# Kernel tuning notes

Hardware: AMD Instinct MI355X
Metric: run time of the kernel (lower is better)

Reference implementation:

```python
import jax, jax.numpy as jnp
import numpy as np

EPS = 1e-7
K_CURV = 1.0                       # init_curvature buffer
HOPFIELD_DIM = 128
BETA = 1.0 / HOPFIELD_DIM ** 0.5   # default beta = 1/sqrt(hopfield_dim)


def _to_tangent0(x):
    # prepend zero time coordinate, clip max norm to 3.5
    zeros = jnp.zeros(x.shape[:-1] + (1,), dtype=x.dtype)
    x = jnp.concatenate([zeros, x], axis=-1)
    n = jnp.linalg.norm(x, axis=-1, keepdims=True)
    factor = jnp.minimum(3.5 / (n + EPS), 1.0)
    return x * factor


def _linner(u, v):
    # Minkowski (Lorentz) inner product: -u0*v0 + sum_i ui*vi
    return -u[..., 0] * v[..., 0] + jnp.sum(u[..., 1:] * v[..., 1:], axis=-1)


def _expmap0(u, k):
    # exp map at hyperboloid origin; u has zero time component
    sk = jnp.sqrt(k)
    xs = u[..., 1:]
    n = jnp.maximum(jnp.linalg.norm(xs, axis=-1, keepdims=True), EPS)
    t = n / sk
    return jnp.concatenate([sk * jnp.cosh(t), sk * jnp.sinh(t) * xs / n], axis=-1)


def _logmap(x, y, k):
    # log map of y in tangent space at x
    xy = _linner(x, y)[..., None]
    dist = jnp.sqrt(k) * jnp.arccosh(jnp.maximum(-xy / k, 1.0 + EPS))
    nomin = y + (xy / k) * x
    denom = jnp.sqrt(jnp.maximum(_linner(nomin, nomin)[..., None], EPS))
    return dist * nomin / denom


def _expmap(x, u, k):
    # exp map of tangent vector u at base point x
    sk = jnp.sqrt(k)
    un = jnp.sqrt(jnp.maximum(_linner(u, u)[..., None], EPS))
    t = un / sk
    return jnp.cosh(t) * x + sk * jnp.sinh(t) * u / un


def _logmap0(x, k):
    # log map at origin; time component of the result is zero
    sk = jnp.sqrt(k)
    xs = x[..., 1:]
    n = jnp.maximum(jnp.linalg.norm(xs, axis=-1, keepdims=True), EPS)
    dist = sk * jnp.arccosh(jnp.maximum(x[..., :1] / sk, 1.0 + EPS))
    return jnp.concatenate([jnp.zeros_like(x[..., :1]), dist * xs / n], axis=-1)


def setup_inputs() -> dict:
    key = jax.random.key(0)
    k1, k2, k3, k4, k5 = jax.random.split(key, 5)
    N, M, D_MEM, D_H, D_OUT = 1024, 2048, 512, 128, 128
    return {
        "queries": jax.random.normal(k1, (N, D_H), dtype=jnp.float32),
        "keys": jax.random.normal(k2, (M, D_MEM), dtype=jnp.float32),
        "values": jax.random.normal(k3, (M, D_MEM), dtype=jnp.float32),
        "W_K": jax.random.normal(k4, (D_MEM, D_H), dtype=jnp.float32) * 0.05,
        "W_V": jax.random.normal(k5, (D_H, D_OUT), dtype=jnp.float32) * 0.05,
    }


def reference(queries, keys, values, W_K, W_V):
    k = K_CURV
    Q = _expmap0(_to_tangent0(queries), k)              # [N, D+1]
    K = _expmap0(_to_tangent0(keys @ W_K), k)           # [M, D+1]
    V = _expmap0(_to_tangent0((values @ W_K) @ W_V), k) # [M, D+1]
    sim = _linner(Q[:, None, :], K[None, :, :])         # [N, M]
    alpha = jax.nn.softmax(-BETA * sim, axis=-1)        # [N, M]
    log_values = _logmap(Q[:, None, :], V[None, :, :], k)  # [N, M, D+1]
    tangent_mean = jnp.sum(alpha[..., None] * log_values, axis=1)  # [N, D+1]
    z = _expmap(Q, tangent_mean, k)
    return _logmap0(z, k)[..., 1:]                      # [N, D]
```

## Files before the change

kernel.cpp:

```cpp
#include <hip/hip_runtime.h>
#include <math.h>

#define EPSF 1e-7f
#define BETA_F 0.08838834764831845f

typedef __attribute__((ext_vector_type(8))) short bf8_t;
typedef __attribute__((ext_vector_type(4))) float f32x4;

#define WS_QT    0
#define WS_LQ    1024
#define WS_KT    2048
#define WS_VTM   4096
#define WS_LV    6144
#define WS_QS    8192
#define WS_QHI   139264
#define WS_QLO   204800
#define WS_KHI   270336
#define WS_KLO   401408
#define WS_VHI   532480
#define WS_VLO   663552
#define WS_VTHI  794624
#define WS_VTLO  925696
#define WS_WKT0  1056768
#define WS_WKT1  1089536
#define WS_WKT2  1122304
#define WS_WVT0  1155072
#define WS_WVT1  1163264
#define WS_WVT2  1171456
#define WS_PART  1179648

__device__ __forceinline__ float wave_sum(float v) {
#pragma unroll
  for (int off = 32; off > 0; off >>= 1) v += __shfl_xor(v, off);
  return v;
}
__device__ __forceinline__ unsigned short f2bf(float x) {
  unsigned int u = __float_as_uint(x);
  u += 0x7FFFu + ((u >> 16) & 1u);
  return (unsigned short)(u >> 16);
}
__device__ __forceinline__ float bf2f(unsigned short h) {
  return __uint_as_float(((unsigned int)h) << 16);
}
__device__ __forceinline__ void split3(float x, unsigned short& s0, unsigned short& s1,
                                       unsigned short& s2) {
  s0 = f2bf(x);
  float r1 = x - bf2f(s0);
  s1 = f2bf(r1);
  s2 = f2bf(r1 - bf2f(s1));
}
__device__ __forceinline__ bf8_t ld8(const unsigned short* p) {
  return __builtin_bit_cast(bf8_t, *(const uint4*)p);
}
__device__ __forceinline__ f32x4 mfma16(bf8_t a, bf8_t b, f32x4 c) {
  return __builtin_amdgcn_mfma_f32_16x16x32_bf16(a, b, c, 0, 0, 0);
}

__global__ void prep_q(const float* __restrict__ queries, float* __restrict__ Qs,
                       float* __restrict__ qt, float* __restrict__ lqv,
                       unsigned int* __restrict__ Qhi, unsigned int* __restrict__ Qlo) {
  int i = blockIdx.x;
  int lane = threadIdx.x;
  float2 r = ((const float2*)(queries + (size_t)i * 128))[lane];
  float s2 = wave_sum(r.x * r.x + r.y * r.y);
  float n = sqrtf(s2);
  float f = fminf(3.5f / (n + EPSF), 1.0f);
  float t = fmaxf(n * f, EPSF);
  float coef = sinhf(t) / t * f;
  float ch = coshf(t);
  float x0 = coef * r.x, x1 = coef * r.y;
  ((float2*)(Qs + (size_t)i * 128))[lane] = make_float2(x0, x1);
  unsigned short h0 = f2bf(x0), h1 = f2bf(x1);
  Qhi[i * 64 + lane] = (unsigned)h0 | ((unsigned)h1 << 16);
  unsigned short g0 = f2bf(x0 - bf2f(h0)), g1 = f2bf(x1 - bf2f(h1));
  Qlo[i * 64 + lane] = (unsigned)g0 | ((unsigned)g1 << 16);
  if (lane == 0) {
    qt[i] = ch;
    lqv[i] = coef * coef * s2 - ch * ch;
  }
}

__global__ void convert_w(const float* __restrict__ WK, const float* __restrict__ WV,
                          unsigned short* __restrict__ WKT0, unsigned short* __restrict__ WKT1,
                          unsigned short* __restrict__ WKT2,
                          unsigned short* __restrict__ WVT0, unsigned short* __restrict__ WVT1,
                          unsigned short* __restrict__ WVT2) {
  int t = blockIdx.x * 256 + threadIdx.x;
  if (t < 65536) {
    int n = t >> 9, k = t & 511;
    unsigned short a, b, c;
    split3(WK[k * 128 + n], a, b, c);
    WKT0[t] = a; WKT1[t] = b; WKT2[t] = c;
  } else {
    int t2 = t - 65536;
    int n = t2 >> 7, k = t2 & 127;
    unsigned short a, b, c;
    split3(WV[k * 128 + n], a, b, c);
    WVT0[t2] = a; WVT1[t2] = b; WVT2[t2] = c;
  }
}

__launch_bounds__(512, 2)
__global__ void prep_kv(const float* __restrict__ keys, const float* __restrict__ values,
                        const unsigned short* __restrict__ WKT0,
                        const unsigned short* __restrict__ WKT1,
                        const unsigned short* __restrict__ WKT2,
                        const unsigned short* __restrict__ WVT0,
                        const unsigned short* __restrict__ WVT1,
                        const unsigned short* __restrict__ WVT2,
                        unsigned short* __restrict__ Khi, unsigned short* __restrict__ Klo,
                        float* __restrict__ kt,
                        unsigned short* __restrict__ Vhi, unsigned short* __restrict__ Vlo,
                        unsigned short* __restrict__ VThi, unsigned short* __restrict__ VTlo,
                        float* __restrict__ vt, float* __restrict__ lv) {
  int tid = threadIdx.x, wv = tid >> 6, lane = tid & 63;
  int l15 = lane & 15, lh = lane >> 4;
  int b = blockIdx.x;
  bool isK = b < 128;
  int r0 = (b & 127) * 16;
  const float* src = isK ? keys : values;

  __shared__ __align__(16) float ldsD[16][132];
  __shared__ __align__(16) unsigned short v1p[3][16][128];
  __shared__ __align__(16) float ldsD2[16][132];
  __shared__ __align__(16) float ldsT[128][17];

  f32x4 acc = f32x4{0, 0, 0, 0};
  const float* arow = src + (size_t)(r0 + l15) * 512 + lh * 8;
  size_t bbase = (size_t)(wv * 16 + l15) * 512 + lh * 8;

  float4 pa0[2], pa1[2];
  bf8_t pb0[2], pb1[2], pb2[2];
  pa0[0] = *(const float4*)(arow);
  pa1[0] = *(const float4*)(arow + 4);
  pb0[0] = ld8(WKT0 + bbase);
  pb1[0] = ld8(WKT1 + bbase);
  pb2[0] = ld8(WKT2 + bbase);
  pa0[1] = *(const float4*)(arow + 32);
  pa1[1] = *(const float4*)(arow + 36);
  pb0[1] = ld8(WKT0 + bbase + 32);
  pb1[1] = ld8(WKT1 + bbase + 32);
  pb2[1] = ld8(WKT2 + bbase + 32);
  __builtin_amdgcn_sched_barrier(0);

#pragma unroll
  for (int ks = 0; ks < 16; ++ks) {
    const int cur = ks & 1;
    float4 a0 = pa0[cur], a1 = pa1[cur];
    bf8_t b0 = pb0[cur], b1 = pb1[cur], b2 = pb2[cur];
    if (ks < 14) {
      pa0[cur] = *(const float4*)(arow + (ks + 2) * 32);
      pa1[cur] = *(const float4*)(arow + (ks + 2) * 32 + 4);
      pb0[cur] = ld8(WKT0 + bbase + (ks + 2) * 32);
      pb1[cur] = ld8(WKT1 + bbase + (ks + 2) * 32);
      pb2[cur] = ld8(WKT2 + bbase + (ks + 2) * 32);
    }
    __builtin_amdgcn_sched_barrier(0);
    float av[8] = {a0.x, a0.y, a0.z, a0.w, a1.x, a1.y, a1.z, a1.w};
    bf8_t aa0, aa1, aa2;
#pragma unroll
    for (int i = 0; i < 8; ++i) {
      unsigned short p0, p1, p2;
      split3(av[i], p0, p1, p2);
      aa0[i] = (short)p0; aa1[i] = (short)p1; aa2[i] = (short)p2;
    }
    acc = mfma16(aa0, b0, acc);
    acc = mfma16(aa0, b1, acc);
    acc = mfma16(aa1, b0, acc);
    acc = mfma16(aa0, b2, acc);
    acc = mfma16(aa1, b1, acc);
    acc = mfma16(aa2, b0, acc);
  }
#pragma unroll
  for (int r = 0; r < 4; ++r) ldsD[lh * 4 + r][wv * 16 + l15] = acc[r];
  __syncthreads();

  if (isK) {
    if (tid < 256) {
      int row = tid >> 4, l = tid & 15;
      float a[8];
#pragma unroll
      for (int n = 0; n < 8; ++n) a[n] = ldsD[row][n * 16 + l];
      float s2 = 0.f;
#pragma unroll
      for (int n = 0; n < 8; ++n) s2 += a[n] * a[n];
#pragma unroll
      for (int off = 1; off < 16; off <<= 1) s2 += __shfl_xor(s2, off);
      float nn = sqrtf(s2);
      float f = fminf(3.5f / (nn + EPSF), 1.0f);
      float t = fmaxf(nn * f, EPSF);
      float coef = sinhf(t) / t * f;
      if (l == 0) kt[r0 + row] = coshf(t);
#pragma unroll
      for (int n = 0; n < 8; ++n) {
        float sv = coef * a[n];
        unsigned short h = f2bf(sv);
        Khi[(size_t)(r0 + row) * 128 + n * 16 + l] = h;
        Klo[(size_t)(r0 + row) * 128 + n * 16 + l] = f2bf(sv - bf2f(h));
      }
    }
    return;
  }

  if (tid < 256) {
    int row = tid >> 4, l = tid & 15;
#pragma unroll
    for (int n = 0; n < 8; ++n) {
      unsigned short p0, p1, p2;
      split3(ldsD[row][n * 16 + l], p0, p1, p2);
      v1p[0][row][n * 16 + l] = p0;
      v1p[1][row][n * 16 + l] = p1;
      v1p[2][row][n * 16 + l] = p2;
    }
  }
  __syncthreads();

  f32x4 a2 = f32x4{0, 0, 0, 0};
  size_t b2base = (size_t)(wv * 16 + l15) * 128 + lh * 8;
  bf8_t qb0[2], qb1[2], qb2[2];
  qb0[0] = ld8(WVT0 + b2base);
  qb1[0] = ld8(WVT1 + b2base);
  qb2[0] = ld8(WVT2 + b2base);
  __builtin_amdgcn_sched_barrier(0);
#pragma unroll
  for (int ks = 0; ks < 4; ++ks) {
    const int cur = ks & 1;
    bf8_t b0 = qb0[cur], b1 = qb1[cur], b2 = qb2[cur];
    if (ks < 3) {
      qb0[cur ^ 1] = ld8(WVT0 + b2base + (ks + 1) * 32);
      qb1[cur ^ 1] = ld8(WVT1 + b2base + (ks + 1) * 32);
      qb2[cur ^ 1] = ld8(WVT2 + b2base + (ks + 1) * 32);
    }
    __builtin_amdgcn_sched_barrier(0);
    bf8_t x0 = ld8(&v1p[0][l15][ks * 32 + lh * 8]);
    bf8_t x1 = ld8(&v1p[1][l15][ks * 32 + lh * 8]);
    bf8_t x2 = ld8(&v1p[2][l15][ks * 32 + lh * 8]);
    a2 = mfma16(x0, b0, a2);
    a2 = mfma16(x0, b1, a2);
    a2 = mfma16(x1, b0, a2);
    a2 = mfma16(x0, b2, a2);
    a2 = mfma16(x1, b1, a2);
    a2 = mfma16(x2, b0, a2);
  }
#pragma unroll
  for (int r = 0; r < 4; ++r) ldsD2[lh * 4 + r][wv * 16 + l15] = a2[r];
  __syncthreads();

  if (tid < 256) {
    int row = tid >> 4, l = tid & 15;
    float a[8];
#pragma unroll
    for (int n = 0; n < 8; ++n) a[n] = ldsD2[row][n * 16 + l];
    float s2 = 0.f;
#pragma unroll
    for (int n = 0; n < 8; ++n) s2 += a[n] * a[n];
#pragma unroll
    for (int off = 1; off < 16; off <<= 1) s2 += __shfl_xor(s2, off);
    float nn = sqrtf(s2);
    float f = fminf(3.5f / (nn + EPSF), 1.0f);
    float t = fmaxf(nn * f, EPSF);
    float coef = sinhf(t) / t * f;
    float ch = coshf(t);
    if (l == 0) {
      vt[r0 + row] = ch;
      lv[r0 + row] = coef * coef * s2 - ch * ch;
    }
#pragma unroll
    for (int n = 0; n < 8; ++n) {
      float sv = coef * a[n];
      unsigned short h = f2bf(sv);
      Vhi[(size_t)(r0 + row) * 128 + n * 16 + l] = h;
      Vlo[(size_t)(r0 + row) * 128 + n * 16 + l] = f2bf(sv - bf2f(h));
      ldsT[n * 16 + l][row] = sv;
    }
  }
  __syncthreads();

  if (tid < 128) {
    int d = tid;
    unsigned int wh[8], wl[8];
#pragma unroll
    for (int i = 0; i < 8; ++i) {
      float s0 = ldsT[d][2 * i], s1 = ldsT[d][2 * i + 1];
      unsigned short h0 = f2bf(s0), h1 = f2bf(s1);
      unsigned short g0 = f2bf(s0 - bf2f(h0)), g1 = f2bf(s1 - bf2f(h1));
      wh[i] = (unsigned)h0 | ((unsigned)h1 << 16);
      wl[i] = (unsigned)g0 | ((unsigned)g1 << 16);
    }
    size_t o = (size_t)d * 2048 + r0;
    *(uint4*)(VThi + o) = make_uint4(wh[0], wh[1], wh[2], wh[3]);
    *(uint4*)(VThi + o + 8) = make_uint4(wh[4], wh[5], wh[6], wh[7]);
    *(uint4*)(VTlo + o) = make_uint4(wl[0], wl[1], wl[2], wl[3]);
    *(uint4*)(VTlo + o + 8) = make_uint4(wl[4], wl[5], wl[6], wl[7]);
  }
}

__launch_bounds__(256, 2)
__global__ void attn_mfma(const unsigned short* __restrict__ Qhi, const unsigned short* __restrict__ Qlo,
                          const unsigned short* __restrict__ Khi, const unsigned short* __restrict__ Klo,
                          const unsigned short* __restrict__ Vhi, const unsigned short* __restrict__ Vlo,
                          const unsigned short* __restrict__ VThi, const unsigned short* __restrict__ VTlo,
                          const float* __restrict__ qt, const float* __restrict__ lqv,
                          const float* __restrict__ kt, const float* __restrict__ vt,
                          const float* __restrict__ lv, float* __restrict__ part) {
  int tid = threadIdx.x, wv = tid >> 6, lane = tid & 63;
  int l15 = lane & 15, lh = lane >> 4;
  int qg = blockIdx.x >> 3, sp = blockIdx.x & 7;
  int q0 = qg * 16;
  int j0 = sp * 256 + wv * 64;

  __shared__ __align__(16) unsigned short ghA[4][1024];
  __shared__ __align__(16) unsigned short glA[4][1024];
  __shared__ __align__(16) float mergeO[4][16][132];
  __shared__ float mergeS[4][3][16];

  bf8_t qfh[4], qfl[4];
  {
    const unsigned short* qp = Qhi + (size_t)(q0 + l15) * 128 + lh * 8;
    const unsigned short* ql = Qlo + (size_t)(q0 + l15) * 128 + lh * 8;
#pragma unroll
    for (int ks = 0; ks < 4; ++ks) { qfh[ks] = ld8(qp + ks * 32); qfl[ks] = ld8(ql + ks * 32); }
  }
  float qtr[4], lq2[4];
#pragma unroll
  for (int r = 0; r < 4; ++r) {
    int q = q0 + lh * 4 + r;
    qtr[r] = qt[q];
    lq2[r] = 2.0f + lqv[q];
  }
  float ktj[4], vtj[4], lvj[4];
#pragma unroll
  for (int n = 0; n < 4; ++n) {
    int j = j0 + n * 16 + l15;
    ktj[n] = kt[j]; vtj[n] = vt[j]; lvj[n] = lv[j];
  }

  auto loadT = [&](bf8_t* st, int nn) {
    size_t jrow = (size_t)(j0 + nn * 16 + l15) * 128 + lh * 8;
#pragma unroll
    for (int ks = 0; ks < 4; ++ks) {
      st[ks * 4 + 0] = ld8(Khi + jrow + ks * 32);
      st[ks * 4 + 1] = ld8(Klo + jrow + ks * 32);
      st[ks * 4 + 2] = ld8(Vhi + jrow + ks * 32);
      st[ks * 4 + 3] = ld8(Vlo + jrow + ks * 32);
    }
  };
  auto mfmaT = [&](const bf8_t* st, f32x4& s, f32x4& c) {
#pragma unroll
    for (int ks = 0; ks < 4; ++ks) {
      s = mfma16(qfh[ks], st[ks * 4 + 0], s);
      s = mfma16(qfh[ks], st[ks * 4 + 1], s);
      s = mfma16(qfl[ks], st[ks * 4 + 0], s);
      c = mfma16(qfh[ks], st[ks * 4 + 2], c);
      c = mfma16(qfh[ks], st[ks * 4 + 3], c);
      c = mfma16(qfl[ks], st[ks * 4 + 2], c);
    }
  };
  f32x4 sf[4], cf[4];
#pragma unroll
  for (int n = 0; n < 4; ++n) { sf[n] = f32x4{0, 0, 0, 0}; cf[n] = f32x4{0, 0, 0, 0}; }
  bf8_t stA[16], stB[16];
  loadT(stA, 0);
  loadT(stB, 1);
  mfmaT(stA, sf[0], cf[0]);
  loadT(stA, 2);
  mfmaT(stB, sf[1], cf[1]);
  loadT(stB, 3);
  mfmaT(stA, sf[2], cf[2]);
  mfmaT(stB, sf[3], cf[3]);

  bf8_t vA[16], vB[16];
  auto loadV = [&](bf8_t* st, int jk) {
#pragma unroll
    for (int dn = 0; dn < 8; ++dn) {
      size_t vrow = (size_t)(dn * 16 + l15) * 2048 + j0 + jk * 32 + lh * 8;
      st[dn * 2 + 0] = ld8(VThi + vrow);
      st[dn * 2 + 1] = ld8(VTlo + vrow);
    }
  };
  loadV(vA, 0);

  float lsum[4] = {0, 0, 0, 0}, tcs[4] = {0, 0, 0, 0}, tts[4] = {0, 0, 0, 0};
#pragma unroll
  for (int n = 0; n < 4; ++n) {
#pragma unroll
    for (int r = 0; r < 4; ++r) {
      float sim = sf[n][r] - qtr[r] * ktj[n];
      float c = cf[n][r] - qtr[r] * vtj[n];
      float e = expf(-BETA_F * sim);
      float z = fmaxf(-c, 1.0f + EPSF);
      float dist = acoshf(z);
      float den2 = fmaxf(lvj[n] + lq2[r] * c * c, EPSF);
      float g = e * dist * rsqrtf(den2);
      lsum[r] += e;
      tcs[r] += g * c;
      tts[r] += g * vtj[n];
      unsigned short gh = f2bf(g);
      unsigned short gl = f2bf(g - bf2f(gh));
      int q_ = lh * 4 + r;
      int idx = (q_ * 64 + n * 16 + l15) ^ ((q_ & 7) << 3);
      ghA[wv][idx] = gh;
      glA[wv][idx] = gl;
    }
  }
  loadV(vB, 1);
  asm volatile("s_waitcnt lgkmcnt(0)" ::: "memory");
  __builtin_amdgcn_sched_barrier(0);

  f32x4 accO[8];
#pragma unroll
  for (int dn = 0; dn < 8; ++dn) accO[dn] = f32x4{0, 0, 0, 0};
  {
    int base0 = (l15 * 64 + 0 * 32 + lh * 8) ^ ((l15 & 7) << 3);
    bf8_t ah = ld8(&ghA[wv][base0]);
    bf8_t al = ld8(&glA[wv][base0]);
#pragma unroll
    for (int dn = 0; dn < 8; ++dn) {
      accO[dn] = mfma16(ah, vA[dn * 2 + 0], accO[dn]);
      accO[dn] = mfma16(ah, vA[dn * 2 + 1], accO[dn]);
      accO[dn] = mfma16(al, vA[dn * 2 + 0], accO[dn]);
    }
  }
  {
    int base1 = (l15 * 64 + 1 * 32 + lh * 8) ^ ((l15 & 7) << 3);
    bf8_t ah = ld8(&ghA[wv][base1]);
    bf8_t al = ld8(&glA[wv][base1]);
#pragma unroll
    for (int dn = 0; dn < 8; ++dn) {
      accO[dn] = mfma16(ah, vB[dn * 2 + 0], accO[dn]);
      accO[dn] = mfma16(ah, vB[dn * 2 + 1], accO[dn]);
      accO[dn] = mfma16(al, vB[dn * 2 + 0], accO[dn]);
    }
  }

#pragma unroll
  for (int r = 0; r < 4; ++r) {
#pragma unroll
    for (int off = 1; off < 16; off <<= 1) {
      lsum[r] += __shfl_xor(lsum[r], off);
      tcs[r] += __shfl_xor(tcs[r], off);
      tts[r] += __shfl_xor(tts[r], off);
    }
  }

#pragma unroll
  for (int r = 0; r < 4; ++r) {
    int q_ = lh * 4 + r;
#pragma unroll
    for (int dn = 0; dn < 8; ++dn) mergeO[wv][q_][dn * 16 + l15] = accO[dn][r];
    if (l15 == 0) {
      mergeS[wv][0][q_] = lsum[r];
      mergeS[wv][1][q_] = tcs[r];
      mergeS[wv][2][q_] = tts[r];
    }
  }
  __syncthreads();

#pragma unroll
  for (int e = 0; e < 2; ++e) {
    int t = tid + e * 256;
    int q_ = t >> 5, d0 = (t & 31) * 4;
    float4 s = make_float4(0.f, 0.f, 0.f, 0.f);
#pragma unroll
    for (int w = 0; w < 4; ++w) {
      float4 v = *(const float4*)&mergeO[w][q_][d0];
      s.x += v.x; s.y += v.y; s.z += v.z; s.w += v.w;
    }
    float* P = part + ((size_t)(q0 + q_) * 8 + sp) * 132;
    *(float4*)(P + d0) = s;
  }
  if (tid < 16) {
    int q_ = tid;
    float a = 0, b = 0, cc2 = 0;
#pragma unroll
    for (int w = 0; w < 4; ++w) {
      a += mergeS[w][0][q_];
      b += mergeS[w][1][q_];
      cc2 += mergeS[w][2][q_];
    }
    float* P = part + ((size_t)(q0 + q_) * 8 + sp) * 132;
    P[128] = a; P[129] = b; P[130] = cc2;
  }
}

__global__ void merge_fin(const float* __restrict__ part, const float* __restrict__ Qs,
                          const float* __restrict__ qt, float* __restrict__ out) {
  int qi = blockIdx.x;
  int lane = threadIdx.x;
  const float* P = part + (size_t)qi * 8 * 132;
  float ox = 0, oy = 0, l = 0, tc = 0, tt = 0;
#pragma unroll
  for (int s = 0; s < 8; ++s) {
    const float* p = P + s * 132;
    float2 o2 = *(const float2*)(p + 2 * lane);
    ox += o2.x; oy += o2.y;
    l += p[128]; tc += p[129]; tt += p[130];
  }
  float2 q2 = ((const float2*)(Qs + (size_t)qi * 128))[lane];
  float qtv = qt[qi];
  float invl = 1.0f / l;
  float Tmx = (ox + tc * q2.x) * invl;
  float Tmy = (oy + tc * q2.y) * invl;
  float Tmt = (tt + tc * qtv) * invl;
  float sp2 = wave_sum(Tmx * Tmx + Tmy * Tmy);
  float LT = sp2 - Tmt * Tmt;
  float un = sqrtf(fmaxf(LT, EPSF));
  float ch = coshf(un);
  float shv = sinhf(un) / un;
  float zx = ch * q2.x + shv * Tmx;
  float zy = ch * q2.y + shv * Tmy;
  float zt = ch * qtv + shv * Tmt;
  float zn2 = wave_sum(zx * zx + zy * zy);
  float nz = fmaxf(sqrtf(zn2), EPSF);
  float dist = acoshf(fmaxf(zt, 1.0f + EPSF));
  float sc = dist / nz;
  ((float2*)(out + (size_t)qi * 128))[lane] = make_float2(sc * zx, sc * zy);
}

extern "C" void kernel_launch(void* const* d_in, const int* in_sizes, int n_in,
                              void* d_out, int out_size, void* d_ws, size_t ws_size,
                              hipStream_t stream) {
  const float* queries = (const float*)d_in[0];
  const float* keys = (const float*)d_in[1];
  const float* values = (const float*)d_in[2];
  const float* WK = (const float*)d_in[3];
  const float* WV = (const float*)d_in[4];
  float* ws = (float*)d_ws;

  float* qt_ = ws + WS_QT;
  float* lq_ = ws + WS_LQ;
  float* kt_ = ws + WS_KT;
  float* vt_ = ws + WS_VTM;
  float* lv_ = ws + WS_LV;
  float* Qs = ws + WS_QS;
  unsigned short* Qhi = (unsigned short*)(ws + WS_QHI);
  unsigned short* Qlo = (unsigned short*)(ws + WS_QLO);
  unsigned short* Khi = (unsigned short*)(ws + WS_KHI);
  unsigned short* Klo = (unsigned short*)(ws + WS_KLO);
  unsigned short* Vhi = (unsigned short*)(ws + WS_VHI);
  unsigned short* Vlo = (unsigned short*)(ws + WS_VLO);
  unsigned short* VThi = (unsigned short*)(ws + WS_VTHI);
  unsigned short* VTlo = (unsigned short*)(ws + WS_VTLO);
  unsigned short* WKT0 = (unsigned short*)(ws + WS_WKT0);
  unsigned short* WKT1 = (unsigned short*)(ws + WS_WKT1);
  unsigned short* WKT2 = (unsigned short*)(ws + WS_WKT2);
  unsigned short* WVT0 = (unsigned short*)(ws + WS_WVT0);
  unsigned short* WVT1 = (unsigned short*)(ws + WS_WVT1);
  unsigned short* WVT2 = (unsigned short*)(ws + WS_WVT2);
  float* part = ws + WS_PART;
  float* out = (float*)d_out;

  prep_q<<<1024, 64, 0, stream>>>(queries, Qs, qt_, lq_, (unsigned int*)Qhi, (unsigned int*)Qlo);
  convert_w<<<320, 256, 0, stream>>>(WK, WV, WKT0, WKT1, WKT2, WVT0, WVT1, WVT2);
  prep_kv<<<256, 512, 0, stream>>>(keys, values, WKT0, WKT1, WKT2, WVT0, WVT1, WVT2,
                                   Khi, Klo, kt_, Vhi, Vlo, VThi, VTlo, vt_, lv_);
  attn_mfma<<<512, 256, 0, stream>>>(Qhi, Qlo, Khi, Klo, Vhi, Vlo, VThi, VTlo,
                                     qt_, lq_, kt_, vt_, lv_, part);
  merge_fin<<<1024, 64, 0, stream>>>(part, Qs, qt_, out);
}
```

Baseline: 70.57 us.

## Fuse prep_q with weight conversion and merge finalize into attention via atomic counter

```diff
diff --git a/kernel.cpp b/kernel.cpp
--- a/kernel.cpp
+++ b/kernel.cpp
@@ -28,6 +28,7 @@
 #define WS_WVT1  1163264
 #define WS_WVT2  1171456
 #define WS_PART  1179648
+#define WS_CTR   2260992
 
 __device__ __forceinline__ float wave_sum(float v) {
 #pragma unroll
@@ -56,11 +57,35 @@
   return __builtin_amdgcn_mfma_f32_16x16x32_bf16(a, b, c, 0, 0, 0);
 }
 
-__global__ void prep_q(const float* __restrict__ queries, float* __restrict__ Qs,
-                       float* __restrict__ qt, float* __restrict__ lqv,
-                       unsigned int* __restrict__ Qhi, unsigned int* __restrict__ Qlo) {
-  int i = blockIdx.x;
-  int lane = threadIdx.x;
+__global__ void prep_wq(const float* __restrict__ queries,
+                        const float* __restrict__ WK, const float* __restrict__ WV,
+                        float* __restrict__ Qs, float* __restrict__ qt, float* __restrict__ lqv,
+                        unsigned int* __restrict__ Qhi, unsigned int* __restrict__ Qlo,
+                        unsigned short* __restrict__ WKT0, unsigned short* __restrict__ WKT1,
+                        unsigned short* __restrict__ WKT2,
+                        unsigned short* __restrict__ WVT0, unsigned short* __restrict__ WVT1,
+                        unsigned short* __restrict__ WVT2,
+                        unsigned int* __restrict__ ctr) {
+  int b = blockIdx.x, tid = threadIdx.x;
+  if (b < 320) {
+    int t = b * 256 + tid;
+    if (t < 65536) {
+      int n = t >> 9, k = t & 511;
+      unsigned short a, bb, c;
+      split3(WK[k * 128 + n], a, bb, c);
+      WKT0[t] = a; WKT1[t] = bb; WKT2[t] = c;
+    } else {
+      int t2 = t - 65536;
+      int n = t2 >> 7, k = t2 & 127;
+      unsigned short a, bb, c;
+      split3(WV[k * 128 + n], a, bb, c);
+      WVT0[t2] = a; WVT1[t2] = bb; WVT2[t2] = c;
+    }
+    return;
+  }
+  if (b == 320 && tid < 64) ctr[tid] = 0;
+  int wv = tid >> 6, lane = tid & 63;
+  int i = (b - 320) * 4 + wv;
   float2 r = ((const float2*)(queries + (size_t)i * 128))[lane];
   float s2 = wave_sum(r.x * r.x + r.y * r.y);
   float n = sqrtf(s2);
@@ -77,26 +102,6 @@
   if (lane == 0) {
     qt[i] = ch;
     lqv[i] = coef * coef * s2 - ch * ch;
-  }
-}
-
-__global__ void convert_w(const float* __restrict__ WK, const float* __restrict__ WV,
-                          unsigned short* __restrict__ WKT0, unsigned short* __restrict__ WKT1,
-                          unsigned short* __restrict__ WKT2,
-                          unsigned short* __restrict__ WVT0, unsigned short* __restrict__ WVT1,
-                          unsigned short* __restrict__ WVT2) {
-  int t = blockIdx.x * 256 + threadIdx.x;
-  if (t < 65536) {
-    int n = t >> 9, k = t & 511;
-    unsigned short a, b, c;
-    split3(WK[k * 128 + n], a, b, c);
-    WKT0[t] = a; WKT1[t] = b; WKT2[t] = c;
-  } else {
-    int t2 = t - 65536;
-    int n = t2 >> 7, k = t2 & 127;
-    unsigned short a, b, c;
-    split3(WV[k * 128 + n], a, b, c);
-    WVT0[t2] = a; WVT1[t2] = b; WVT2[t2] = c;
   }
 }
 
@@ -302,7 +307,9 @@
                           const unsigned short* __restrict__ VThi, const unsigned short* __restrict__ VTlo,
                           const float* __restrict__ qt, const float* __restrict__ lqv,
                           const float* __restrict__ kt, const float* __restrict__ vt,
-                          const float* __restrict__ lv, float* __restrict__ part) {
+                          const float* __restrict__ lv, float* __restrict__ part,
+                          const float* __restrict__ Qs, float* __restrict__ out,
+                          unsigned int* __restrict__ ctr) {
   int tid = threadIdx.x, wv = tid >> 6, lane = tid & 63;
   int l15 = lane & 15, lh = lane >> 4;
   int qg = blockIdx.x >> 3, sp = blockIdx.x & 7;
@@ -481,40 +488,50 @@
     float* P = part + ((size_t)(q0 + q_) * 8 + sp) * 132;
     P[128] = a; P[129] = b; P[130] = cc2;
   }
-}
-
-__global__ void merge_fin(const float* __restrict__ part, const float* __restrict__ Qs,
-                          const float* __restrict__ qt, float* __restrict__ out) {
-  int qi = blockIdx.x;
-  int lane = threadIdx.x;
-  const float* P = part + (size_t)qi * 8 * 132;
-  float ox = 0, oy = 0, l = 0, tc = 0, tt = 0;
-#pragma unroll
-  for (int s = 0; s < 8; ++s) {
-    const float* p = P + s * 132;
-    float2 o2 = *(const float2*)(p + 2 * lane);
-    ox += o2.x; oy += o2.y;
-    l += p[128]; tc += p[129]; tt += p[130];
-  }
-  float2 q2 = ((const float2*)(Qs + (size_t)qi * 128))[lane];
-  float qtv = qt[qi];
-  float invl = 1.0f / l;
-  float Tmx = (ox + tc * q2.x) * invl;
-  float Tmy = (oy + tc * q2.y) * invl;
-  float Tmt = (tt + tc * qtv) * invl;
-  float sp2 = wave_sum(Tmx * Tmx + Tmy * Tmy);
-  float LT = sp2 - Tmt * Tmt;
-  float un = sqrtf(fmaxf(LT, EPSF));
-  float ch = coshf(un);
-  float shv = sinhf(un) / un;
-  float zx = ch * q2.x + shv * Tmx;
-  float zy = ch * q2.y + shv * Tmy;
-  float zt = ch * qtv + shv * Tmt;
-  float zn2 = wave_sum(zx * zx + zy * zy);
-  float nz = fmaxf(sqrtf(zn2), EPSF);
-  float dist = acoshf(fmaxf(zt, 1.0f + EPSF));
-  float sc = dist / nz;
-  ((float2*)(out + (size_t)qi * 128))[lane] = make_float2(sc * zx, sc * zy);
+
+  __threadfence();
+  __shared__ int lastFlag;
+  if (tid == 0) {
+    unsigned int old = atomicAdd(&ctr[qg], 1u);
+    lastFlag = (old == 7u) ? 1 : 0;
+  }
+  __syncthreads();
+  if (lastFlag) {
+    __threadfence();
+    if (tid == 0) ctr[qg] = 0;
+#pragma unroll
+    for (int e = 0; e < 4; ++e) {
+      int qi = q0 + wv * 4 + e;
+      const float* P = part + (size_t)qi * 8 * 132;
+      float ox = 0, oy = 0, l = 0, tc = 0, tt = 0;
+#pragma unroll
+      for (int s = 0; s < 8; ++s) {
+        const float* p = P + s * 132;
+        float2 o2 = *(const float2*)(p + 2 * lane);
+        ox += o2.x; oy += o2.y;
+        l += p[128]; tc += p[129]; tt += p[130];
+      }
+      float2 q2 = ((const float2*)(Qs + (size_t)qi * 128))[lane];
+      float qtv = qt[qi];
+      float invl = 1.0f / l;
+      float Tmx = (ox + tc * q2.x) * invl;
+      float Tmy = (oy + tc * q2.y) * invl;
+      float Tmt = (tt + tc * qtv) * invl;
+      float sp2 = wave_sum(Tmx * Tmx + Tmy * Tmy);
+      float LT = sp2 - Tmt * Tmt;
+      float un = sqrtf(fmaxf(LT, EPSF));
+      float ch = coshf(un);
+      float shv = sinhf(un) / un;
+      float zx = ch * q2.x + shv * Tmx;
+      float zy = ch * q2.y + shv * Tmy;
+      float zt = ch * qtv + shv * Tmt;
+      float zn2 = wave_sum(zx * zx + zy * zy);
+      float nz = fmaxf(sqrtf(zn2), EPSF);
+      float dist = acoshf(fmaxf(zt, 1.0f + EPSF));
+      float sc = dist / nz;
+      ((float2*)(out + (size_t)qi * 128))[lane] = make_float2(sc * zx, sc * zy);
+    }
+  }
 }
 
 extern "C" void kernel_launch(void* const* d_in, const int* in_sizes, int n_in,
@@ -548,13 +565,14 @@
   unsigned short* WVT1 = (unsigned short*)(ws + WS_WVT1);
   unsigned short* WVT2 = (unsigned short*)(ws + WS_WVT2);
   float* part = ws + WS_PART;
+  unsigned int* ctr = (unsigned int*)(ws + WS_CTR);
   float* out = (float*)d_out;
 
-  prep_q<<<1024, 64, 0, stream>>>(queries, Qs, qt_, lq_, (unsigned int*)Qhi, (unsigned int*)Qlo);
-  convert_w<<<320, 256, 0, stream>>>(WK, WV, WKT0, WKT1, WKT2, WVT0, WVT1, WVT2);
+  prep_wq<<<576, 256, 0, stream>>>(queries, WK, WV, Qs, qt_, lq_,
+                                   (unsigned int*)Qhi, (unsigned int*)Qlo,
+                                   WKT0, WKT1, WKT2, WVT0, WVT1, WVT2, ctr);
   prep_kv<<<256, 512, 0, stream>>>(keys, values, WKT0, WKT1, WKT2, WVT0, WVT1, WVT2,
                                    Khi, Klo, kt_, Vhi, Vlo, VThi, VTlo, vt_, lv_);
   attn_mfma<<<512, 256, 0, stream>>>(Qhi, Qlo, Khi, Klo, Vhi, Vlo, VThi, VTlo,
-                                     qt_, lq_, kt_, vt_, lv_, part);
-  merge_fin<<<1024, 64, 0, stream>>>(part, Qs, qt_, out);
-}
+                                     qt_, lq_, kt_, vt_, lv_, part, Qs, out, ctr);
+}
```

Result: slower. 141.2 us (+100.1%).

## Fold query and weight preprocessing into consumer kernels to cut launches

Applied to the files above, without the earlier changes.

```diff
diff --git a/kernel.cpp b/kernel.cpp
--- a/kernel.cpp
+++ b/kernel.cpp
@@ -7,27 +7,16 @@
 typedef __attribute__((ext_vector_type(8))) short bf8_t;
 typedef __attribute__((ext_vector_type(4))) float f32x4;
 
-#define WS_QT    0
-#define WS_LQ    1024
-#define WS_KT    2048
-#define WS_VTM   4096
-#define WS_LV    6144
-#define WS_QS    8192
-#define WS_QHI   139264
-#define WS_QLO   204800
-#define WS_KHI   270336
-#define WS_KLO   401408
-#define WS_VHI   532480
-#define WS_VLO   663552
-#define WS_VTHI  794624
-#define WS_VTLO  925696
-#define WS_WKT0  1056768
-#define WS_WKT1  1089536
-#define WS_WKT2  1122304
-#define WS_WVT0  1155072
-#define WS_WVT1  1163264
-#define WS_WVT2  1171456
-#define WS_PART  1179648
+#define WS_KT    0
+#define WS_VTM   2048
+#define WS_LV    4096
+#define WS_KHI   6144
+#define WS_KLO   137216
+#define WS_VHI   268288
+#define WS_VLO   399360
+#define WS_VTHI  530432
+#define WS_VTLO  661504
+#define WS_PART  792576
 
 __device__ __forceinline__ float wave_sum(float v) {
 #pragma unroll
@@ -56,69 +45,21 @@
   return __builtin_amdgcn_mfma_f32_16x16x32_bf16(a, b, c, 0, 0, 0);
 }
 
-__global__ void prep_q(const float* __restrict__ queries, float* __restrict__ Qs,
-                       float* __restrict__ qt, float* __restrict__ lqv,
-                       unsigned int* __restrict__ Qhi, unsigned int* __restrict__ Qlo) {
-  int i = blockIdx.x;
-  int lane = threadIdx.x;
-  float2 r = ((const float2*)(queries + (size_t)i * 128))[lane];
-  float s2 = wave_sum(r.x * r.x + r.y * r.y);
-  float n = sqrtf(s2);
-  float f = fminf(3.5f / (n + EPSF), 1.0f);
-  float t = fmaxf(n * f, EPSF);
-  float coef = sinhf(t) / t * f;
-  float ch = coshf(t);
-  float x0 = coef * r.x, x1 = coef * r.y;
-  ((float2*)(Qs + (size_t)i * 128))[lane] = make_float2(x0, x1);
-  unsigned short h0 = f2bf(x0), h1 = f2bf(x1);
-  Qhi[i * 64 + lane] = (unsigned)h0 | ((unsigned)h1 << 16);
-  unsigned short g0 = f2bf(x0 - bf2f(h0)), g1 = f2bf(x1 - bf2f(h1));
-  Qlo[i * 64 + lane] = (unsigned)g0 | ((unsigned)g1 << 16);
-  if (lane == 0) {
-    qt[i] = ch;
-    lqv[i] = coef * coef * s2 - ch * ch;
-  }
-}
-
-__global__ void convert_w(const float* __restrict__ WK, const float* __restrict__ WV,
-                          unsigned short* __restrict__ WKT0, unsigned short* __restrict__ WKT1,
-                          unsigned short* __restrict__ WKT2,
-                          unsigned short* __restrict__ WVT0, unsigned short* __restrict__ WVT1,
-                          unsigned short* __restrict__ WVT2) {
-  int t = blockIdx.x * 256 + threadIdx.x;
-  if (t < 65536) {
-    int n = t >> 9, k = t & 511;
-    unsigned short a, b, c;
-    split3(WK[k * 128 + n], a, b, c);
-    WKT0[t] = a; WKT1[t] = b; WKT2[t] = c;
-  } else {
-    int t2 = t - 65536;
-    int n = t2 >> 7, k = t2 & 127;
-    unsigned short a, b, c;
-    split3(WV[k * 128 + n], a, b, c);
-    WVT0[t2] = a; WVT1[t2] = b; WVT2[t2] = c;
-  }
-}
-
 __launch_bounds__(512, 2)
-__global__ void prep_kv(const float* __restrict__ keys, const float* __restrict__ values,
-                        const unsigned short* __restrict__ WKT0,
-                        const unsigned short* __restrict__ WKT1,
-                        const unsigned short* __restrict__ WKT2,
-                        const unsigned short* __restrict__ WVT0,
-                        const unsigned short* __restrict__ WVT1,
-                        const unsigned short* __restrict__ WVT2,
-                        unsigned short* __restrict__ Khi, unsigned short* __restrict__ Klo,
-                        float* __restrict__ kt,
-                        unsigned short* __restrict__ Vhi, unsigned short* __restrict__ Vlo,
-                        unsigned short* __restrict__ VThi, unsigned short* __restrict__ VTlo,
-                        float* __restrict__ vt, float* __restrict__ lv) {
+__global__ void prep_kv_w(const float* __restrict__ keys, const float* __restrict__ values,
+                          const float* __restrict__ WK, const float* __restrict__ WV,
+                          unsigned short* __restrict__ Khi, unsigned short* __restrict__ Klo,
+                          float* __restrict__ kt,
+                          unsigned short* __restrict__ Vhi, unsigned short* __restrict__ Vlo,
+                          unsigned short* __restrict__ VThi, unsigned short* __restrict__ VTlo,
+                          float* __restrict__ vt, float* __restrict__ lv) {
   int tid = threadIdx.x, wv = tid >> 6, lane = tid & 63;
   int l15 = lane & 15, lh = lane >> 4;
   int b = blockIdx.x;
   bool isK = b < 128;
   int r0 = (b & 127) * 16;
   const float* src = isK ? keys : values;
+  int ncol = wv * 16 + l15;
 
   __shared__ __align__(16) float ldsD[16][132];
   __shared__ __align__(16) unsigned short v1p[3][16][128];
@@ -127,33 +68,32 @@
 
   f32x4 acc = f32x4{0, 0, 0, 0};
   const float* arow = src + (size_t)(r0 + l15) * 512 + lh * 8;
-  size_t bbase = (size_t)(wv * 16 + l15) * 512 + lh * 8;
 
   float4 pa0[2], pa1[2];
-  bf8_t pb0[2], pb1[2], pb2[2];
+  float wkb[2][8];
   pa0[0] = *(const float4*)(arow);
   pa1[0] = *(const float4*)(arow + 4);
-  pb0[0] = ld8(WKT0 + bbase);
-  pb1[0] = ld8(WKT1 + bbase);
-  pb2[0] = ld8(WKT2 + bbase);
+#pragma unroll
+  for (int i = 0; i < 8; ++i) wkb[0][i] = WK[(size_t)(lh * 8 + i) * 128 + ncol];
   pa0[1] = *(const float4*)(arow + 32);
   pa1[1] = *(const float4*)(arow + 36);
-  pb0[1] = ld8(WKT0 + bbase + 32);
-  pb1[1] = ld8(WKT1 + bbase + 32);
-  pb2[1] = ld8(WKT2 + bbase + 32);
+#pragma unroll
+  for (int i = 0; i < 8; ++i) wkb[1][i] = WK[(size_t)(32 + lh * 8 + i) * 128 + ncol];
   __builtin_amdgcn_sched_barrier(0);
 
 #pragma unroll
   for (int ks = 0; ks < 16; ++ks) {
     const int cur = ks & 1;
     float4 a0 = pa0[cur], a1 = pa1[cur];
-    bf8_t b0 = pb0[cur], b1 = pb1[cur], b2 = pb2[cur];
+    float wb[8];
+#pragma unroll
+    for (int i = 0; i < 8; ++i) wb[i] = wkb[cur][i];
     if (ks < 14) {
       pa0[cur] = *(const float4*)(arow + (ks + 2) * 32);
       pa1[cur] = *(const float4*)(arow + (ks + 2) * 32 + 4);
-      pb0[cur] = ld8(WKT0 + bbase + (ks + 2) * 32);
-      pb1[cur] = ld8(WKT1 + bbase + (ks + 2) * 32);
-      pb2[cur] = ld8(WKT2 + bbase + (ks + 2) * 32);
+#pragma unroll
+      for (int i = 0; i < 8; ++i)
+        wkb[cur][i] = WK[(size_t)((ks + 2) * 32 + lh * 8 + i) * 128 + ncol];
     }
     __builtin_amdgcn_sched_barrier(0);
     float av[8] = {a0.x, a0.y, a0.z, a0.w, a1.x, a1.y, a1.z, a1.w};
@@ -164,12 +104,19 @@
       split3(av[i], p0, p1, p2);
       aa0[i] = (short)p0; aa1[i] = (short)p1; aa2[i] = (short)p2;
     }
-    acc = mfma16(aa0, b0, acc);
-    acc = mfma16(aa0, b1, acc);
-    acc = mfma16(aa1, b0, acc);
-    acc = mfma16(aa0, b2, acc);
-    acc = mfma16(aa1, b1, acc);
-    acc = mfma16(aa2, b0, acc);
+    bf8_t bb0, bb1, bb2;
+#pragma unroll
+    for (int i = 0; i < 8; ++i) {
+      unsigned short p0, p1, p2;
+      split3(wb[i], p0, p1, p2);
+      bb0[i] = (short)p0; bb1[i] = (short)p1; bb2[i] = (short)p2;
+    }
+    acc = mfma16(aa0, bb0, acc);
+    acc = mfma16(aa0, bb1, acc);
+    acc = mfma16(aa1, bb0, acc);
+    acc = mfma16(aa0, bb2, acc);
+    acc = mfma16(aa1, bb1, acc);
+    acc = mfma16(aa2, bb0, acc);
   }
 #pragma unroll
   for (int r = 0; r < 4; ++r) ldsD[lh * 4 + r][wv * 16 + l15] = acc[r];
@@ -216,31 +163,38 @@
   __syncthreads();
 
   f32x4 a2 = f32x4{0, 0, 0, 0};
-  size_t b2base = (size_t)(wv * 16 + l15) * 128 + lh * 8;
-  bf8_t qb0[2], qb1[2], qb2[2];
-  qb0[0] = ld8(WVT0 + b2base);
-  qb1[0] = ld8(WVT1 + b2base);
-  qb2[0] = ld8(WVT2 + b2base);
+  float wvb[2][8];
+#pragma unroll
+  for (int i = 0; i < 8; ++i) wvb[0][i] = WV[(size_t)(lh * 8 + i) * 128 + ncol];
   __builtin_amdgcn_sched_barrier(0);
 #pragma unroll
   for (int ks = 0; ks < 4; ++ks) {
     const int cur = ks & 1;
-    bf8_t b0 = qb0[cur], b1 = qb1[cur], b2 = qb2[cur];
+    float wb[8];
+#pragma unroll
+    for (int i = 0; i < 8; ++i) wb[i] = wvb[cur][i];
     if (ks < 3) {
-      qb0[cur ^ 1] = ld8(WVT0 + b2base + (ks + 1) * 32);
-      qb1[cur ^ 1] = ld8(WVT1 + b2base + (ks + 1) * 32);
-      qb2[cur ^ 1] = ld8(WVT2 + b2base + (ks + 1) * 32);
+#pragma unroll
+      for (int i = 0; i < 8; ++i)
+        wvb[cur ^ 1][i] = WV[(size_t)((ks + 1) * 32 + lh * 8 + i) * 128 + ncol];
     }
     __builtin_amdgcn_sched_barrier(0);
+    bf8_t bb0, bb1, bb2;
+#pragma unroll
+    for (int i = 0; i < 8; ++i) {
+      unsigned short p0, p1, p2;
+      split3(wb[i], p0, p1, p2);
+      bb0[i] = (short)p0; bb1[i] = (short)p1; bb2[i] = (short)p2;
+    }
     bf8_t x0 = ld8(&v1p[0][l15][ks * 32 + lh * 8]);
     bf8_t x1 = ld8(&v1p[1][l15][ks * 32 + lh * 8]);
     bf8_t x2 = ld8(&v1p[2][l15][ks * 32 + lh * 8]);
-    a2 = mfma16(x0, b0, a2);
-    a2 = mfma16(x0, b1, a2);
-    a2 = mfma16(x1, b0, a2);
-    a2 = mfma16(x0, b2, a2);
-    a2 = mfma16(x1, b1, a2);
-    a2 = mfma16(x2, b0, a2);
+    a2 = mfma16(x0, bb0, a2);
+    a2 = mfma16(x0, bb1, a2);
+    a2 = mfma16(x1, bb0, a2);
+    a2 = mfma16(x0, bb2, a2);
+    a2 = mfma16(x1, bb1, a2);
+    a2 = mfma16(x2, bb0, a2);
   }
 #pragma unroll
   for (int r = 0; r < 4; ++r) ldsD2[lh * 4 + r][wv * 16 + l15] = a2[r];
@@ -296,11 +250,10 @@
 }
 
 __launch_bounds__(256, 2)
-__global__ void attn_mfma(const unsigned short* __restrict__ Qhi, const unsigned short* __restrict__ Qlo,
+__global__ void attn_mfma(const float* __restrict__ queries,
                           const unsigned short* __restrict__ Khi, const unsigned short* __restrict__ Klo,
                           const unsigned short* __restrict__ Vhi, const unsigned short* __restrict__ Vlo,
                           const unsigned short* __restrict__ VThi, const unsigned short* __restrict__ VTlo,
-                          const float* __restrict__ qt, const float* __restrict__ lqv,
                           const float* __restrict__ kt, const float* __restrict__ vt,
                           const float* __restrict__ lv, float* __restrict__ part) {
   int tid = threadIdx.x, wv = tid >> 6, lane = tid & 63;
@@ -309,24 +262,50 @@
   int q0 = qg * 16;
   int j0 = sp * 256 + wv * 64;
 
+  __shared__ __align__(16) unsigned short qtH[16][128];
+  __shared__ __align__(16) unsigned short qtL[16][128];
+  __shared__ float qtS[16], lqS[16];
   __shared__ __align__(16) unsigned short ghA[4][1024];
   __shared__ __align__(16) unsigned short glA[4][1024];
   __shared__ __align__(16) float mergeO[4][16][132];
   __shared__ float mergeS[4][3][16];
 
+#pragma unroll
+  for (int e = 0; e < 4; ++e) {
+    int row = wv * 4 + e;
+    int i = q0 + row;
+    float2 r = ((const float2*)(queries + (size_t)i * 128))[lane];
+    float s2q = wave_sum(r.x * r.x + r.y * r.y);
+    float nq = sqrtf(s2q);
+    float fq = fminf(3.5f / (nq + EPSF), 1.0f);
+    float tq = fmaxf(nq * fq, EPSF);
+    float coefq = sinhf(tq) / tq * fq;
+    float chq = coshf(tq);
+    float x0 = coefq * r.x, x1 = coefq * r.y;
+    unsigned short h0 = f2bf(x0), h1 = f2bf(x1);
+    qtH[row][2 * lane] = h0;
+    qtH[row][2 * lane + 1] = h1;
+    unsigned short g0 = f2bf(x0 - bf2f(h0)), g1 = f2bf(x1 - bf2f(h1));
+    qtL[row][2 * lane] = g0;
+    qtL[row][2 * lane + 1] = g1;
+    if (lane == 0) {
+      qtS[row] = chq;
+      lqS[row] = coefq * coefq * s2q - chq * chq;
+    }
+  }
+  __syncthreads();
+
   bf8_t qfh[4], qfl[4];
-  {
-    const unsigned short* qp = Qhi + (size_t)(q0 + l15) * 128 + lh * 8;
-    const unsigned short* ql = Qlo + (size_t)(q0 + l15) * 128 + lh * 8;
-#pragma unroll
-    for (int ks = 0; ks < 4; ++ks) { qfh[ks] = ld8(qp + ks * 32); qfl[ks] = ld8(ql + ks * 32); }
+#pragma unroll
+  for (int ks = 0; ks < 4; ++ks) {
+    qfh[ks] = ld8(&qtH[l15][lh * 8 + ks * 32]);
+    qfl[ks] = ld8(&qtL[l15][lh * 8 + ks * 32]);
   }
   float qtr[4], lq2[4];
 #pragma unroll
   for (int r = 0; r < 4; ++r) {
-    int q = q0 + lh * 4 + r;
-    qtr[r] = qt[q];
-    lq2[r] = 2.0f + lqv[q];
+    qtr[r] = qtS[lh * 4 + r];
+    lq2[r] = 2.0f + lqS[lh * 4 + r];
   }
   float ktj[4], vtj[4], lvj[4];
 #pragma unroll
@@ -483,8 +462,8 @@
   }
 }
 
-__global__ void merge_fin(const float* __restrict__ part, const float* __restrict__ Qs,
-                          const float* __restrict__ qt, float* __restrict__ out) {
+__global__ void merge_fin(const float* __restrict__ part, const float* __restrict__ queries,
+                          float* __restrict__ out) {
   int qi = blockIdx.x;
   int lane = threadIdx.x;
   const float* P = part + (size_t)qi * 8 * 132;
@@ -496,19 +475,25 @@
     ox += o2.x; oy += o2.y;
     l += p[128]; tc += p[129]; tt += p[130];
   }
-  float2 q2 = ((const float2*)(Qs + (size_t)qi * 128))[lane];
-  float qtv = qt[qi];
+  float2 rq = ((const float2*)(queries + (size_t)qi * 128))[lane];
+  float s2q = wave_sum(rq.x * rq.x + rq.y * rq.y);
+  float nq = sqrtf(s2q);
+  float fq = fminf(3.5f / (nq + EPSF), 1.0f);
+  float tq = fmaxf(nq * fq, EPSF);
+  float coefq = sinhf(tq) / tq * fq;
+  float qtv = coshf(tq);
+  float qx = coefq * rq.x, qy = coefq * rq.y;
   float invl = 1.0f / l;
-  float Tmx = (ox + tc * q2.x) * invl;
-  float Tmy = (oy + tc * q2.y) * invl;
+  float Tmx = (ox + tc * qx) * invl;
+  float Tmy = (oy + tc * qy) * invl;
   float Tmt = (tt + tc * qtv) * invl;
   float sp2 = wave_sum(Tmx * Tmx + Tmy * Tmy);
   float LT = sp2 - Tmt * Tmt;
   float un = sqrtf(fmaxf(LT, EPSF));
   float ch = coshf(un);
   float shv = sinhf(un) / un;
-  float zx = ch * q2.x + shv * Tmx;
-  float zy = ch * q2.y + shv * Tmy;
+  float zx = ch * qx + shv * Tmx;
+  float zy = ch * qy + shv * Tmy;
   float zt = ch * qtv + shv * Tmt;
   float zn2 = wave_sum(zx * zx + zy * zy);
   float nz = fmaxf(sqrtf(zn2), EPSF);
@@ -527,34 +512,21 @@
   const float* WV = (const float*)d_in[4];
   float* ws = (float*)d_ws;
 
-  float* qt_ = ws + WS_QT;
-  float* lq_ = ws + WS_LQ;
   float* kt_ = ws + WS_KT;
   float* vt_ = ws + WS_VTM;
   float* lv_ = ws + WS_LV;
-  float* Qs = ws + WS_QS;
-  unsigned short* Qhi = (unsigned short*)(ws + WS_QHI);
-  unsigned short* Qlo = (unsigned short*)(ws + WS_QLO);
   unsigned short* Khi = (unsigned short*)(ws + WS_KHI);
   unsigned short* Klo = (unsigned short*)(ws + WS_KLO);
   unsigned short* Vhi = (unsigned short*)(ws + WS_VHI);
   unsigned short* Vlo = (unsigned short*)(ws + WS_VLO);
   unsigned short* VThi = (unsigned short*)(ws + WS_VTHI);
   unsigned short* VTlo = (unsigned short*)(ws + WS_VTLO);
-  unsigned short* WKT0 = (unsigned short*)(ws + WS_WKT0);
-  unsigned short* WKT1 = (unsigned short*)(ws + WS_WKT1);
-  unsigned short* WKT2 = (unsigned short*)(ws + WS_WKT2);
-  unsigned short* WVT0 = (unsigned short*)(ws + WS_WVT0);
-  unsigned short* WVT1 = (unsigned short*)(ws + WS_WVT1);
-  unsigned short* WVT2 = (unsigned short*)(ws + WS_WVT2);
   float* part = ws + WS_PART;
   float* out = (float*)d_out;
 
-  prep_q<<<1024, 64, 0, stream>>>(queries, Qs, qt_, lq_, (unsigned int*)Qhi, (unsigned int*)Qlo);
-  convert_w<<<320, 256, 0, stream>>>(WK, WV, WKT0, WKT1, WKT2, WVT0, WVT1, WVT2);
-  prep_kv<<<256, 512, 0, stream>>>(keys, values, WKT0, WKT1, WKT2, WVT0, WVT1, WVT2,
-                                   Khi, Klo, kt_, Vhi, Vlo, VThi, VTlo, vt_, lv_);
-  attn_mfma<<<512, 256, 0, stream>>>(Qhi, Qlo, Khi, Klo, Vhi, Vlo, VThi, VTlo,
-                                     qt_, lq_, kt_, vt_, lv_, part);
-  merge_fin<<<1024, 64, 0, stream>>>(part, Qs, qt_, out);
-}
+  prep_kv_w<<<256, 512, 0, stream>>>(keys, values, WK, WV,
+                                     Khi, Klo, kt_, Vhi, Vlo, VThi, VTlo, vt_, lv_);
+  attn_mfma<<<512, 256, 0, stream>>>(queries, Khi, Klo, Vhi, Vlo, VThi, VTlo,
+                                     kt_, vt_, lv_, part);
+  merge_fin<<<1024, 64, 0, stream>>>(part, queries, out);
+}
```

Measured after the change: 58.42 us (median of 2 runs). 17.2% less time.
